# Optimization experiments

Hardware: AMD Instinct MI355X
Metric: run time of the kernel (lower is better)

## Reference

```python
import jax, jax.numpy as jnp
import numpy as np

TOKENS = 8192
IN_F = 4096
OUT_F = 4096
QMAX = 127.0  # int8 symmetric quant range
EPS = 1e-8


def setup_inputs() -> dict:
    key = jax.random.key(0)
    k1, k2, k3, k4 = jax.random.split(key, 4)
    x = jax.random.normal(k1, (TOKENS, IN_F), dtype=jnp.float32)
    # Pre-quantized int8 weight [out_features, in_features]
    weight_q = jax.random.randint(k2, (OUT_F, IN_F), -127, 128, dtype=jnp.int8)
    # Per-output-channel weight scales (realistic small magnitudes)
    weight_scale = jax.random.uniform(k3, (OUT_F,), dtype=jnp.float32) * 0.01 + 1e-3
    bias = jax.random.normal(k4, (OUT_F,), dtype=jnp.float32)
    return {"x": x, "weight_q": weight_q, "weight_scale": weight_scale, "bias": bias}


def reference(x, weight_q, weight_scale, bias):
    # Dynamic per-token symmetric int8 activation quantization
    absmax = jnp.max(jnp.abs(x), axis=-1, keepdims=True)           # [T, 1]
    x_scale = jnp.maximum(absmax, EPS) / QMAX                      # [T, 1]
    x_q = jnp.clip(jnp.round(x / x_scale), -QMAX, QMAX).astype(jnp.int8)
    acc = jax.lax.dot_general(
        x_q, weight_q,
        dimension_numbers=(((1,), (1,)), ((), ())),
        preferred_element_type=jnp.int32,
    )
    # Inline dequant: per-token activation scale * per-channel weight scale
    out = acc.astype(jnp.float32) * x_scale * weight_scale[None, :]
    out = out + bias[None, :]
    return out
```

## Files before the change

kernel.cpp:

```cpp
#include <hip/hip_runtime.h>
#include <cstdint>
#include <cstddef>

#define TOKENS 8192
#define IN_F   4096
#define OUT_F  4096
#define QMAXF  127.0f
#define EPSF   1e-8f

typedef int i32x4  __attribute__((ext_vector_type(4)));
typedef int i32x16 __attribute__((ext_vector_type(16)));

#define BKB 128
#define NTT (IN_F / BKB)
#define SLOT 65536
#define LDS_TOTAL (2 * SLOT)

__device__ __forceinline__ void gload16(const void* g, void* l) {
    __builtin_amdgcn_global_load_lds(
        (const __attribute__((address_space(1))) void*)g,
        (__attribute__((address_space(3))) void*)l,
        16, 0, 0);
}

__device__ __forceinline__ void bar() {
    asm volatile("" ::: "memory");
    __builtin_amdgcn_s_barrier();
    asm volatile("" ::: "memory");
}

__device__ __forceinline__ int quant1(float v, float inv) {
    int q = (int)rintf(v * inv);
    q = q > 127 ? 127 : q;
    q = q < -127 ? -127 : q;
    return q;
}

__device__ __forceinline__ unsigned int pack4i(int a, int b, int c, int d) {
    return (unsigned int)(a & 255) | ((unsigned int)(b & 255) << 8) |
           ((unsigned int)(c & 255) << 16) | ((unsigned int)(d & 255) << 24);
}

__global__ __launch_bounds__(256) void quant_x_kernel(const float* __restrict__ x,
                                                      signed char* __restrict__ xq,
                                                      float* __restrict__ xscale) {
    const int t   = blockIdx.x;
    const int tid = threadIdx.x;
    const float* xr = x + (size_t)t * IN_F + tid * 16;

    float4 v[4];
    float am = 0.0f;
#pragma unroll
    for (int i = 0; i < 4; ++i) {
        v[i] = ((const float4*)xr)[i];
        am = fmaxf(am, fmaxf(fmaxf(fabsf(v[i].x), fabsf(v[i].y)),
                             fmaxf(fabsf(v[i].z), fabsf(v[i].w))));
    }
#pragma unroll
    for (int off = 32; off >= 1; off >>= 1)
        am = fmaxf(am, __shfl_xor(am, off));

    __shared__ float wmax[4];
    const int wid = tid >> 6, lane = tid & 63;
    if (lane == 0) wmax[wid] = am;
    __syncthreads();
    am = fmaxf(fmaxf(wmax[0], wmax[1]), fmaxf(wmax[2], wmax[3]));

    const float s   = fmaxf(am, EPSF) / QMAXF;
    const float inv = QMAXF / fmaxf(am, EPSF);
    if (tid == 0) xscale[t] = s;

    unsigned int w[4];
#pragma unroll
    for (int i = 0; i < 4; ++i) {
        w[i] = pack4i(quant1(v[i].x, inv), quant1(v[i].y, inv),
                      quant1(v[i].z, inv), quant1(v[i].w, inv));
    }
    *(uint4*)(xq + (size_t)t * IN_F + tid * 16) = make_uint4(w[0], w[1], w[2], w[3]);
}

__global__ __launch_bounds__(256) void pack_w_kernel(const int* __restrict__ w,
                                                     signed char* __restrict__ wq) {
    const size_t idx = (size_t)blockIdx.x * 256 + threadIdx.x;
    const int4* src = (const int4*)w + idx * 4;
    unsigned int o[4];
#pragma unroll
    for (int i = 0; i < 4; ++i) {
        int4 u = src[i];
        o[i] = pack4i(u.x, u.y, u.z, u.w);
    }
    ((uint4*)wq)[idx] = make_uint4(o[0], o[1], o[2], o[3]);
}

__global__ __launch_bounds__(512, 2) void gemm_kernel(const signed char* __restrict__ xq,
                                                      const signed char* __restrict__ wq,
                                                      const float* __restrict__ xscale,
                                                      const float* __restrict__ wscale,
                                                      const float* __restrict__ bias,
                                                      float* __restrict__ out) {
    extern __shared__ __align__(16) char lds[];

    const int tid  = threadIdx.x;
    const int wid  = tid >> 6;
    const int lane = tid & 63;
    const int wr   = wid >> 2;
    const int wc   = wid & 3;

    const int bid = blockIdx.x;
    const int swz = (bid & 7) * 64 + (bid >> 3);
    const int bm0 = (swz >> 4) * 256;
    const int bn0 = (swz & 15) * 256;

    const int srow = ((tid >> 7) << 4) + (tid & 15);
    const int skb  = ((tid >> 6) & 1) * 64 + (((tid >> 4) & 3) << 4);
    const signed char* pA = xq + (size_t)(bm0 + srow) * IN_F + skb;
    const signed char* pB = wq + (size_t)(bn0 + srow) * IN_F + skb;
    const int ldst = tid * 16;

    const int l31 = lane & 31, hi = lane >> 5;
    int a_off[4][4], b_off[2][4];
#pragma unroll
    for (int mi = 0; mi < 4; ++mi) {
        const int row = wr * 128 + mi * 32 + l31;
#pragma unroll
        for (int ks = 0; ks < 4; ++ks)
            a_off[mi][ks] = (row >> 4) * 2048 + (ks >> 1) * 1024 +
                            (((ks & 1) * 2 + hi) << 8) + (row & 15) * 16;
    }
#pragma unroll
    for (int ni = 0; ni < 2; ++ni) {
        const int row = wc * 64 + ni * 32 + l31;
#pragma unroll
        for (int ks = 0; ks < 4; ++ks)
            b_off[ni][ks] = 32768 + (row >> 4) * 2048 + (ks >> 1) * 1024 +
                            (((ks & 1) * 2 + hi) << 8) + (row & 15) * 16;
    }

    i32x16 acc[4][2];
#pragma unroll
    for (int mi = 0; mi < 4; ++mi)
#pragma unroll
        for (int ni = 0; ni < 2; ++ni)
#pragma unroll
            for (int r = 0; r < 16; ++r) acc[mi][ni][r] = 0;

#pragma unroll
    for (int c = 0; c < 4; ++c)
        gload16(pA + (size_t)c * 64 * IN_F, lds + c * 8192 + ldst);
#pragma unroll
    for (int c = 0; c < 4; ++c)
        gload16(pB + (size_t)c * 64 * IN_F, lds + 32768 + c * 8192 + ldst);
    asm volatile("s_waitcnt vmcnt(0)" ::: "memory");
    bar();

    for (int t = 0; t < NTT; ++t) {
        const char* S = lds + (t & 1) * SLOT;

        if (t + 1 < NTT) {
            char* D = lds + ((t + 1) & 1) * SLOT;
            const int ko = (t + 1) * BKB;
#pragma unroll
            for (int c = 0; c < 4; ++c)
                gload16(pA + (size_t)c * 64 * IN_F + ko, D + c * 8192 + ldst);
#pragma unroll
            for (int c = 0; c < 4; ++c)
                gload16(pB + (size_t)c * 64 * IN_F + ko, D + 32768 + c * 8192 + ldst);
        }

#pragma unroll
        for (int kh = 0; kh < 2; ++kh) {
            i32x4 a[4][2], b[2][2];
#pragma unroll
            for (int mi = 0; mi < 4; ++mi)
#pragma unroll
                for (int k2 = 0; k2 < 2; ++k2)
                    a[mi][k2] = *(const i32x4*)(S + a_off[mi][kh * 2 + k2]);
#pragma unroll
            for (int ni = 0; ni < 2; ++ni)
#pragma unroll
                for (int k2 = 0; k2 < 2; ++k2)
                    b[ni][k2] = *(const i32x4*)(S + b_off[ni][kh * 2 + k2]);

            __builtin_amdgcn_s_setprio(1);
#pragma unroll
            for (int k2 = 0; k2 < 2; ++k2)
#pragma unroll
                for (int mi = 0; mi < 4; ++mi)
#pragma unroll
                    for (int ni = 0; ni < 2; ++ni)
                        acc[mi][ni] = __builtin_amdgcn_mfma_i32_32x32x32_i8(
                            a[mi][k2], b[ni][k2], acc[mi][ni], 0, 0, 0);
            __builtin_amdgcn_s_setprio(0);
        }

        asm volatile("s_waitcnt vmcnt(0)" ::: "memory");
        bar();
    }

#pragma unroll
    for (int mi = 0; mi < 4; ++mi) {
        const int rbase = bm0 + wr * 128 + mi * 32 + 4 * hi;
        float xsv[16];
#pragma unroll
        for (int r = 0; r < 16; ++r)
            xsv[r] = xscale[rbase + (r & 3) + 8 * (r >> 2)];
#pragma unroll
        for (int ni = 0; ni < 2; ++ni) {
            const int col = bn0 + wc * 64 + ni * 32 + l31;
            const float wsc = wscale[col];
            const float bv  = bias[col];
#pragma unroll
            for (int r = 0; r < 16; ++r) {
                const int row = rbase + (r & 3) + 8 * (r >> 2);
                out[(size_t)row * OUT_F + col] = (float)acc[mi][ni][r] * xsv[r] * wsc + bv;
            }
        }
    }
}

extern "C" void kernel_launch(void* const* d_in, const int* in_sizes, int n_in,
                              void* d_out, int out_size, void* d_ws, size_t ws_size,
                              hipStream_t stream) {
    const float* x      = (const float*)d_in[0];
    const int*   w      = (const int*)d_in[1];
    const float* wscale = (const float*)d_in[2];
    const float* bias   = (const float*)d_in[3];
    float* out = (float*)d_out;

    char* ws = (char*)d_ws;
    signed char* xq  = (signed char*)ws;
    signed char* wq8 = (signed char*)(ws + (size_t)TOKENS * IN_F);
    float* xscale    = (float*)(ws + (size_t)TOKENS * IN_F + (size_t)OUT_F * IN_F);

    hipFuncSetAttribute((const void*)gemm_kernel,
                        hipFuncAttributeMaxDynamicSharedMemorySize, LDS_TOTAL);

    quant_x_kernel<<<TOKENS, 256, 0, stream>>>(x, xq, xscale);
    pack_w_kernel<<<(OUT_F * (IN_F / 16)) / 256, 256, 0, stream>>>(w, wq8);
    gemm_kernel<<<(TOKENS / 256) * (OUT_F / 256), 512, LDS_TOTAL, stream>>>(
        xq, wq8, xscale, wscale, bias, out);
}
```

Baseline: 215.1 us.

## Restructure int8 GEMM main loop into 4-stage LDS pipeline with 16x16x64 MFMA

```diff
diff --git a/kernel.cpp b/kernel.cpp
--- a/kernel.cpp
+++ b/kernel.cpp
@@ -8,13 +8,11 @@
 #define QMAXF  127.0f
 #define EPSF   1e-8f
 
-typedef int i32x4  __attribute__((ext_vector_type(4)));
-typedef int i32x16 __attribute__((ext_vector_type(16)));
-
-#define BKB 128
-#define NTT (IN_F / BKB)
-#define SLOT 65536
-#define LDS_TOTAL (2 * SLOT)
+typedef int i32x4 __attribute__((ext_vector_type(4)));
+
+#define NIT   32
+#define SLOTB 32768
+#define LDS_TOTAL (4 * SLOTB)
 
 __device__ __forceinline__ void gload16(const void* g, void* l) {
     __builtin_amdgcn_global_load_lds(
@@ -27,6 +25,11 @@
     asm volatile("" ::: "memory");
     __builtin_amdgcn_s_barrier();
     asm volatile("" ::: "memory");
+}
+
+__device__ __forceinline__ void lgkm0_fence() {
+    asm volatile("s_waitcnt lgkmcnt(0)" ::: "memory");
+    __builtin_amdgcn_sched_barrier(0);
 }
 
 __device__ __forceinline__ int quant1(float v, float inv) {
@@ -111,108 +114,153 @@
     const int bm0 = (swz >> 4) * 256;
     const int bn0 = (swz & 15) * 256;
 
-    const int srow = ((tid >> 7) << 4) + (tid & 15);
-    const int skb  = ((tid >> 6) & 1) * 64 + (((tid >> 4) & 3) << 4);
-    const signed char* pA = xq + (size_t)(bm0 + srow) * IN_F + skb;
-    const signed char* pB = wq + (size_t)(bn0 + srow) * IN_F + skb;
+    const int srow = ((tid >> 6) << 4) + (tid & 15);
+    const int sgrn = ((tid >> 4) & 3) << 4;
+    const signed char* pA = xq + (size_t)(bm0 + srow) * IN_F + sgrn;
+    const signed char* pB = wq + (size_t)(bn0 + srow) * IN_F + sgrn;
     const int ldst = tid * 16;
 
-    const int l31 = lane & 31, hi = lane >> 5;
-    int a_off[4][4], b_off[2][4];
-#pragma unroll
-    for (int mi = 0; mi < 4; ++mi) {
-        const int row = wr * 128 + mi * 32 + l31;
-#pragma unroll
-        for (int ks = 0; ks < 4; ++ks)
-            a_off[mi][ks] = (row >> 4) * 2048 + (ks >> 1) * 1024 +
-                            (((ks & 1) * 2 + hi) << 8) + (row & 15) * 16;
-    }
-#pragma unroll
-    for (int ni = 0; ni < 2; ++ni) {
-        const int row = wc * 64 + ni * 32 + l31;
-#pragma unroll
-        for (int ks = 0; ks < 4; ++ks)
-            b_off[ni][ks] = 32768 + (row >> 4) * 2048 + (ks >> 1) * 1024 +
-                            (((ks & 1) * 2 + hi) << 8) + (row & 15) * 16;
-    }
-
-    i32x16 acc[4][2];
-#pragma unroll
-    for (int mi = 0; mi < 4; ++mi)
-#pragma unroll
-        for (int ni = 0; ni < 2; ++ni)
-#pragma unroll
-            for (int r = 0; r < 16; ++r) acc[mi][ni][r] = 0;
-
-#pragma unroll
-    for (int c = 0; c < 4; ++c)
-        gload16(pA + (size_t)c * 64 * IN_F, lds + c * 8192 + ldst);
-#pragma unroll
-    for (int c = 0; c < 4; ++c)
-        gload16(pB + (size_t)c * 64 * IN_F, lds + 32768 + c * 8192 + ldst);
-    asm volatile("s_waitcnt vmcnt(0)" ::: "memory");
+    const int lrd = (lane >> 4) * 256 + (lane & 15) * 16;
+    int a_off[8], b_off[4];
+#pragma unroll
+    for (int mi = 0; mi < 8; ++mi) a_off[mi] = (wr * 8 + mi) * 1024 + lrd;
+#pragma unroll
+    for (int ni = 0; ni < 4; ++ni) b_off[ni] = 16384 + (wc * 4 + ni) * 1024 + lrd;
+
+    i32x4 acc[8][4];
+#pragma unroll
+    for (int mi = 0; mi < 8; ++mi)
+#pragma unroll
+        for (int ni = 0; ni < 4; ++ni)
+#pragma unroll
+            for (int r = 0; r < 4; ++r) acc[mi][ni][r] = 0;
+
+#pragma unroll
+    for (int s = 0; s < 3; ++s) {
+        char* S = lds + s * SLOTB;
+        const int ko = s * 64;
+        gload16(pA + ko,                         S + ldst);
+        gload16(pA + (size_t)128 * IN_F + ko,    S + 8192 + ldst);
+        gload16(pB + ko,                         S + 16384 + ldst);
+        gload16(pB + (size_t)128 * IN_F + ko,    S + 24576 + ldst);
+    }
+    asm volatile("s_waitcnt vmcnt(8)" ::: "memory");
     bar();
 
-    for (int t = 0; t < NTT; ++t) {
-        const char* S = lds + (t & 1) * SLOT;
-
-        if (t + 1 < NTT) {
-            char* D = lds + ((t + 1) & 1) * SLOT;
-            const int ko = (t + 1) * BKB;
-#pragma unroll
-            for (int c = 0; c < 4; ++c)
-                gload16(pA + (size_t)c * 64 * IN_F + ko, D + c * 8192 + ldst);
-#pragma unroll
-            for (int c = 0; c < 4; ++c)
-                gload16(pB + (size_t)c * 64 * IN_F + ko, D + 32768 + c * 8192 + ldst);
-        }
-
-#pragma unroll
-        for (int kh = 0; kh < 2; ++kh) {
-            i32x4 a[4][2], b[2][2];
-#pragma unroll
-            for (int mi = 0; mi < 4; ++mi)
-#pragma unroll
-                for (int k2 = 0; k2 < 2; ++k2)
-                    a[mi][k2] = *(const i32x4*)(S + a_off[mi][kh * 2 + k2]);
-#pragma unroll
-            for (int ni = 0; ni < 2; ++ni)
-#pragma unroll
-                for (int k2 = 0; k2 < 2; ++k2)
-                    b[ni][k2] = *(const i32x4*)(S + b_off[ni][kh * 2 + k2]);
-
-            __builtin_amdgcn_s_setprio(1);
-#pragma unroll
-            for (int k2 = 0; k2 < 2; ++k2)
-#pragma unroll
-                for (int mi = 0; mi < 4; ++mi)
-#pragma unroll
-                    for (int ni = 0; ni < 2; ++ni)
-                        acc[mi][ni] = __builtin_amdgcn_mfma_i32_32x32x32_i8(
-                            a[mi][k2], b[ni][k2], acc[mi][ni], 0, 0, 0);
-            __builtin_amdgcn_s_setprio(0);
-        }
-
-        asm volatile("s_waitcnt vmcnt(0)" ::: "memory");
-        bar();
-    }
-
-#pragma unroll
-    for (int mi = 0; mi < 4; ++mi) {
-        const int rbase = bm0 + wr * 128 + mi * 32 + 4 * hi;
-        float xsv[16];
-#pragma unroll
-        for (int r = 0; r < 16; ++r)
-            xsv[r] = xscale[rbase + (r & 3) + 8 * (r >> 2)];
-#pragma unroll
-        for (int ni = 0; ni < 2; ++ni) {
-            const int col = bn0 + wc * 64 + ni * 32 + l31;
+    for (int t = 0; t < NIT; ++t) {
+        const int h0 = 2 * t;
+        const char* S0 = lds + (h0 & 3) * SLOTB;
+        const char* S1 = lds + ((h0 + 1) & 3) * SLOTB;
+        char* G0 = lds + ((h0 + 3) & 3) * SLOTB;
+        char* G1 = lds + ((h0 + 4) & 3) * SLOTB;
+        const bool st0 = (h0 + 3) < 64;
+        const bool st1 = (h0 + 4) < 64;
+        const int ko0 = (h0 + 3) * 64;
+        const int ko1 = (h0 + 4) * 64;
+
+        i32x4 a[4], b[4];
+
+#pragma unroll
+        for (int ni = 0; ni < 4; ++ni) b[ni] = *(const i32x4*)(S0 + b_off[ni]);
+#pragma unroll
+        for (int mi = 0; mi < 4; ++mi) a[mi] = *(const i32x4*)(S0 + a_off[mi]);
+        if (st0) {
+            gload16(pA + ko0,                      G0 + ldst);
+            gload16(pA + (size_t)128 * IN_F + ko0, G0 + 8192 + ldst);
+        }
+        bar();
+        lgkm0_fence();
+        __builtin_amdgcn_s_setprio(1);
+#pragma unroll
+        for (int mi = 0; mi < 4; ++mi)
+#pragma unroll
+            for (int ni = 0; ni < 4; ++ni)
+                acc[mi][ni] = __builtin_amdgcn_mfma_i32_16x16x64_i8(a[mi], b[ni], acc[mi][ni], 0, 0, 0);
+        __builtin_amdgcn_s_setprio(0);
+        bar();
+
+#pragma unroll
+        for (int mi = 0; mi < 4; ++mi) a[mi] = *(const i32x4*)(S0 + a_off[4 + mi]);
+        if (st0) {
+            gload16(pB + ko0,                      G0 + 16384 + ldst);
+            gload16(pB + (size_t)128 * IN_F + ko0, G0 + 24576 + ldst);
+        }
+        bar();
+        lgkm0_fence();
+        __builtin_amdgcn_s_setprio(1);
+#pragma unroll
+        for (int mi = 0; mi < 4; ++mi)
+#pragma unroll
+            for (int ni = 0; ni < 4; ++ni)
+                acc[4 + mi][ni] = __builtin_amdgcn_mfma_i32_16x16x64_i8(a[mi], b[ni], acc[4 + mi][ni], 0, 0, 0);
+        __builtin_amdgcn_s_setprio(0);
+        if (t < NIT - 1) {
+            asm volatile("s_waitcnt vmcnt(8)" ::: "memory");
+        } else {
+            asm volatile("s_waitcnt vmcnt(0)" ::: "memory");
+        }
+        bar();
+
+#pragma unroll
+        for (int ni = 0; ni < 4; ++ni) b[ni] = *(const i32x4*)(S1 + b_off[ni]);
+#pragma unroll
+        for (int mi = 0; mi < 4; ++mi) a[mi] = *(const i32x4*)(S1 + a_off[mi]);
+        if (st1) {
+            gload16(pA + ko1,                      G1 + ldst);
+            gload16(pA + (size_t)128 * IN_F + ko1, G1 + 8192 + ldst);
+        }
+        bar();
+        lgkm0_fence();
+        __builtin_amdgcn_s_setprio(1);
+#pragma unroll
+        for (int mi = 0; mi < 4; ++mi)
+#pragma unroll
+            for (int ni = 0; ni < 4; ++ni)
+                acc[mi][ni] = __builtin_amdgcn_mfma_i32_16x16x64_i8(a[mi], b[ni], acc[mi][ni], 0, 0, 0);
+        __builtin_amdgcn_s_setprio(0);
+        bar();
+
+#pragma unroll
+        for (int mi = 0; mi < 4; ++mi) a[mi] = *(const i32x4*)(S1 + a_off[4 + mi]);
+        if (st1) {
+            gload16(pB + ko1,                      G1 + 16384 + ldst);
+            gload16(pB + (size_t)128 * IN_F + ko1, G1 + 24576 + ldst);
+        }
+        bar();
+        lgkm0_fence();
+        __builtin_amdgcn_s_setprio(1);
+#pragma unroll
+        for (int mi = 0; mi < 4; ++mi)
+#pragma unroll
+            for (int ni = 0; ni < 4; ++ni)
+                acc[4 + mi][ni] = __builtin_amdgcn_mfma_i32_16x16x64_i8(a[mi], b[ni], acc[4 + mi][ni], 0, 0, 0);
+        __builtin_amdgcn_s_setprio(0);
+        if (t < NIT - 2) {
+            asm volatile("s_waitcnt vmcnt(8)" ::: "memory");
+        } else if (t == NIT - 2) {
+            asm volatile("s_waitcnt vmcnt(4)" ::: "memory");
+        } else {
+            asm volatile("s_waitcnt vmcnt(0)" ::: "memory");
+        }
+        bar();
+    }
+
+    const int l15 = lane & 15, lq = lane >> 4;
+#pragma unroll
+    for (int mi = 0; mi < 8; ++mi) {
+        const int rbase = bm0 + wr * 128 + mi * 16 + lq * 4;
+        float xsv[4];
+#pragma unroll
+        for (int j = 0; j < 4; ++j) xsv[j] = xscale[rbase + j];
+#pragma unroll
+        for (int ni = 0; ni < 4; ++ni) {
+            const int col = bn0 + wc * 64 + ni * 16 + l15;
             const float wsc = wscale[col];
             const float bv  = bias[col];
 #pragma unroll
-            for (int r = 0; r < 16; ++r) {
-                const int row = rbase + (r & 3) + 8 * (r >> 2);
-                out[(size_t)row * OUT_F + col] = (float)acc[mi][ni][r] * xsv[r] * wsc + bv;
+            for (int j = 0; j < 4; ++j) {
+                out[(size_t)(rbase + j) * OUT_F + col] =
+                    (float)acc[mi][ni][j] * xsv[j] * wsc + bv;
             }
         }
     }
```

Result: faster. 199.7 us (-7.2%).
